# Performance work log

Measured on AMD Instinct MI355X. Metric: run time of the kernel, lower is better.

Reference implementation:

```python
import jax, jax.numpy as jnp
import numpy as np


def setup_inputs() -> dict:
    key = jax.random.key(0)
    k1, k2, k3, k4, k5, k6 = jax.random.split(key, 6)
    N, M = 4096, 4096      # data matrix
    K, D = 2048, 1024      # parameter matrix K x K, similarity matrix K x D
    Npair = 128            # size of i/j index subsets
    return {
        "actual": jax.random.normal(k1, (N, M), dtype=jnp.float32),
        "prediction": jax.random.normal(k2, (N, M), dtype=jnp.float32),
        "lamb": jnp.asarray(0.1, dtype=jnp.float32),
        "P": jax.random.normal(k3, (K, K), dtype=jnp.float32),
        "S": jax.random.normal(k4, (K, D), dtype=jnp.float32),
        "i_indices": jax.random.randint(k5, (Npair,), 0, K, dtype=jnp.int64),
        "j_indices": jax.random.randint(k6, (Npair,), 0, K, dtype=jnp.int64),
    }


def _safe_norm_rows(diff):
    # L2 norm over last axis with a zero-safe sqrt (grad is 0 at exactly-0 diffs,
    # matching torch's subgradient convention for .norm()).
    d2 = jnp.sum(diff * diff, axis=-1)
    pos = d2 > 0
    return jnp.sqrt(jnp.where(pos, d2, 1.0)) * pos


def reference(actual, prediction, lamb, P, S, i_indices, j_indices):
    # (p > 0) * clamp(p, min=0) == relu(p)
    Pp = jnp.maximum(P, 0.0)
    # penalty term: ||relu(P)||_F
    penalty = jnp.linalg.norm(Pp)
    # pairwise parameter-similarity penalty:
    # sum_{i in I, j in J} relu(P)[i,j] * || S[i,:] - S[j,:] ||_2
    Si = S[i_indices]                       # [Ni, D]
    Sj = S[j_indices]                       # [Nj, D]
    diff = Si[:, None, :] - Sj[None, :, :]  # [Ni, Nj, D]
    norms = _safe_norm_rows(diff)           # [Ni, Nj]
    Pij = Pp[i_indices[:, None], j_indices[None, :]]  # [Ni, Nj]
    parameter_penalty = jnp.sum(Pij * norms)
    data_term = jnp.linalg.norm(actual - prediction)
    return data_term + lamb * (penalty + parameter_penalty)
```

## Files before the change

kernel.cpp:

```cpp
#include <hip/hip_runtime.h>
#include <math.h>

#define BR 1024
#define BP 1024
#define TPB 256

__device__ __forceinline__ float waveReduceSum(float v) {
    #pragma unroll
    for (int off = 32; off > 0; off >>= 1)
        v += __shfl_down(v, off, 64);
    return v;
}

__global__ __launch_bounds__(256, 8)
void fused_kernel(const float* __restrict__ a,
                  const float* __restrict__ p,
                  const float* __restrict__ Pm,
                  const float* __restrict__ S,
                  const int* __restrict__ ii,
                  const int* __restrict__ jj,
                  float* __restrict__ ws,
                  long nAP, long nP, int Npair, int D, int K)
{
    __shared__ float sm0[4], sm1[4];
    const int wave = threadIdx.x >> 6;
    const int lane = threadIdx.x & 63;
    const int bid  = blockIdx.x;

    if (bid < BP) {
        const int totalPairs = Npair * Npair;
        int base = bid * 16 + wave * 4;
        float local = 0.f;
        #pragma unroll
        for (int q = 0; q < 4; ++q) {
            int pair = base + q;
            if (pair < totalPairs) {
                int i = pair / Npair;
                int j = pair - i * Npair;
                int ri = ii[i];
                int rj = jj[j];
                const float4* Si = (const float4*)(S + (long)ri * D);
                const float4* Sj = (const float4*)(S + (long)rj * D);
                float d2 = 0.f;
                int n4 = D >> 2;
                for (int k = lane; k < n4; k += 64) {
                    float4 x = Si[k];
                    float4 y = Sj[k];
                    float e0 = x.x - y.x;
                    float e1 = x.y - y.y;
                    float e2 = x.z - y.z;
                    float e3 = x.w - y.w;
                    d2 += e0*e0 + e1*e1 + e2*e2 + e3*e3;
                }
                d2 = waveReduceSum(d2);
                if (lane == 0 && d2 > 0.f)
                    local += fmaxf(Pm[(long)ri * K + rj], 0.f) * sqrtf(d2);
            }
        }
        if (lane == 0) sm0[wave] = local;
        __syncthreads();
        if (threadIdx.x == 0)
            ws[2 * BR + bid] = sm0[0] + sm0[1] + sm0[2] + sm0[3];
    } else {
        const int rb = bid - BP;
        const long tid    = (long)rb * TPB + threadIdx.x;
        const long stride = (long)BR * TPB;

        const float4* a4 = (const float4*)a;
        const float4* p4 = (const float4*)p;
        long n4 = nAP >> 2;

        float s0a = 0.f, s0b = 0.f, s0c = 0.f, s0d = 0.f;
        long i = tid;
        for (; i + 3 * stride < n4; i += 4 * stride) {
            float4 av0 = a4[i];
            float4 av1 = a4[i + stride];
            float4 av2 = a4[i + 2 * stride];
            float4 av3 = a4[i + 3 * stride];
            float4 pv0 = p4[i];
            float4 pv1 = p4[i + stride];
            float4 pv2 = p4[i + 2 * stride];
            float4 pv3 = p4[i + 3 * stride];
            {
                float d0 = av0.x - pv0.x, d1 = av0.y - pv0.y;
                float d2 = av0.z - pv0.z, d3 = av0.w - pv0.w;
                s0a += d0*d0 + d1*d1 + d2*d2 + d3*d3;
            }
            {
                float d0 = av1.x - pv1.x, d1 = av1.y - pv1.y;
                float d2 = av1.z - pv1.z, d3 = av1.w - pv1.w;
                s0b += d0*d0 + d1*d1 + d2*d2 + d3*d3;
            }
            {
                float d0 = av2.x - pv2.x, d1 = av2.y - pv2.y;
                float d2 = av2.z - pv2.z, d3 = av2.w - pv2.w;
                s0c += d0*d0 + d1*d1 + d2*d2 + d3*d3;
            }
            {
                float d0 = av3.x - pv3.x, d1 = av3.y - pv3.y;
                float d2 = av3.z - pv3.z, d3 = av3.w - pv3.w;
                s0d += d0*d0 + d1*d1 + d2*d2 + d3*d3;
            }
        }
        for (; i < n4; i += stride) {
            float4 av = a4[i];
            float4 pv = p4[i];
            float d0 = av.x - pv.x, d1 = av.y - pv.y;
            float d2 = av.z - pv.z, d3 = av.w - pv.w;
            s0a += d0*d0 + d1*d1 + d2*d2 + d3*d3;
        }

        const float4* P4 = (const float4*)Pm;
        long nP4 = nP >> 2;
        float s1a = 0.f, s1b = 0.f;
        i = tid;
        for (; i + stride < nP4; i += 2 * stride) {
            float4 v0 = P4[i];
            float4 v1 = P4[i + stride];
            {
                float r0 = fmaxf(v0.x, 0.f), r1 = fmaxf(v0.y, 0.f);
                float r2 = fmaxf(v0.z, 0.f), r3 = fmaxf(v0.w, 0.f);
                s1a += r0*r0 + r1*r1 + r2*r2 + r3*r3;
            }
            {
                float r0 = fmaxf(v1.x, 0.f), r1 = fmaxf(v1.y, 0.f);
                float r2 = fmaxf(v1.z, 0.f), r3 = fmaxf(v1.w, 0.f);
                s1b += r0*r0 + r1*r1 + r2*r2 + r3*r3;
            }
        }
        for (; i < nP4; i += stride) {
            float4 v = P4[i];
            float r0 = fmaxf(v.x, 0.f), r1 = fmaxf(v.y, 0.f);
            float r2 = fmaxf(v.z, 0.f), r3 = fmaxf(v.w, 0.f);
            s1a += r0*r0 + r1*r1 + r2*r2 + r3*r3;
        }

        float s0 = waveReduceSum(s0a + s0b + s0c + s0d);
        float s1 = waveReduceSum(s1a + s1b);
        if (lane == 0) { sm0[wave] = s0; sm1[wave] = s1; }
        __syncthreads();
        if (threadIdx.x == 0) {
            ws[rb]      = sm0[0] + sm0[1] + sm0[2] + sm0[3];
            ws[BR + rb] = sm1[0] + sm1[1] + sm1[2] + sm1[3];
        }
    }
}

__global__ void finalize_kernel(const float* __restrict__ ws,
                                const float* __restrict__ lamb,
                                float* __restrict__ out)
{
    float a0 = 0.f, a1 = 0.f, a2 = 0.f;
    for (int i = threadIdx.x; i < BR; i += TPB) {
        a0 += ws[i];
        a1 += ws[BR + i];
    }
    for (int i = threadIdx.x; i < BP; i += TPB)
        a2 += ws[2 * BR + i];

    a0 = waveReduceSum(a0);
    a1 = waveReduceSum(a1);
    a2 = waveReduceSum(a2);

    __shared__ float m0[4], m1[4], m2[4];
    int wave = threadIdx.x >> 6;
    int lane = threadIdx.x & 63;
    if (lane == 0) { m0[wave] = a0; m1[wave] = a1; m2[wave] = a2; }
    __syncthreads();
    if (threadIdx.x == 0) {
        float A0 = m0[0] + m0[1] + m0[2] + m0[3];
        float A1 = m1[0] + m1[1] + m1[2] + m1[3];
        float A2 = m2[0] + m2[1] + m2[2] + m2[3];
        out[0] = sqrtf(A0) + lamb[0] * (sqrtf(A1) + A2);
    }
}

extern "C" void kernel_launch(void* const* d_in, const int* in_sizes, int n_in,
                              void* d_out, int out_size, void* d_ws, size_t ws_size,
                              hipStream_t stream) {
    const float* actual = (const float*)d_in[0];
    const float* pred   = (const float*)d_in[1];
    const float* lamb   = (const float*)d_in[2];
    const float* Pm     = (const float*)d_in[3];
    const float* S      = (const float*)d_in[4];
    const int*   ii     = (const int*)d_in[5];
    const int*   jj     = (const int*)d_in[6];
    float* out = (float*)d_out;
    float* ws  = (float*)d_ws;

    long nAP   = in_sizes[0];
    long nP    = in_sizes[3];
    int  K     = (int)lround(sqrt((double)nP));
    int  Npair = in_sizes[5];
    int  D     = (int)(in_sizes[4] / K);

    fused_kernel<<<BP + BR, TPB, 0, stream>>>(actual, pred, Pm, S, ii, jj, ws,
                                              nAP, nP, Npair, D, K);
    finalize_kernel<<<1, TPB, 0, stream>>>(ws, lamb, out);
}
```

Measured before the change: 36.37 us.

## Stage Si rows in LDS for pair penalty and widen reduction grid

```diff
diff --git a/kernel.cpp b/kernel.cpp
--- a/kernel.cpp
+++ b/kernel.cpp
@@ -1,9 +1,9 @@
 #include <hip/hip_runtime.h>
 #include <math.h>
 
-#define BR 1024
-#define BP 1024
 #define TPB 256
+#define RB  4096
+#define TI  2
 
 __device__ __forceinline__ float waveReduceSum(float v) {
     #pragma unroll
@@ -12,7 +12,7 @@
     return v;
 }
 
-__global__ __launch_bounds__(256, 8)
+__global__ __launch_bounds__(TPB, 4)
 void fused_kernel(const float* __restrict__ a,
                   const float* __restrict__ p,
                   const float* __restrict__ Pm,
@@ -20,59 +20,77 @@
                   const int* __restrict__ ii,
                   const int* __restrict__ jj,
                   float* __restrict__ ws,
-                  long nAP, long nP, int Npair, int D, int K)
+                  long nAP, long nP, int Npair, int D, int K, int PBn)
 {
-    __shared__ float sm0[4], sm1[4];
     const int wave = threadIdx.x >> 6;
     const int lane = threadIdx.x & 63;
-    const int bid  = blockIdx.x;
-
-    if (bid < BP) {
-        const int totalPairs = Npair * Npair;
-        int base = bid * 16 + wave * 4;
+
+    if ((int)blockIdx.x < PBn) {
+        __shared__ float SiL[TI][1024];
+        __shared__ float psum[4];
+        const int i0 = blockIdx.x * TI;
+        const int n4 = D >> 2;
+
+        for (int idx = threadIdx.x; idx < TI * n4; idx += TPB) {
+            int r = idx / n4, c = idx - r * n4;
+            float4 v = make_float4(0.f, 0.f, 0.f, 0.f);
+            if (i0 + r < Npair)
+                v = ((const float4*)(S + (long)ii[i0 + r] * D))[c];
+            ((float4*)SiL[r])[c] = v;
+        }
+        __syncthreads();
+
+        const int ri0 = (i0     < Npair) ? ii[i0]     : 0;
+        const int ri1 = (i0 + 1 < Npair) ? ii[i0 + 1] : 0;
+
         float local = 0.f;
-        #pragma unroll
-        for (int q = 0; q < 4; ++q) {
-            int pair = base + q;
-            if (pair < totalPairs) {
-                int i = pair / Npair;
-                int j = pair - i * Npair;
-                int ri = ii[i];
-                int rj = jj[j];
-                const float4* Si = (const float4*)(S + (long)ri * D);
-                const float4* Sj = (const float4*)(S + (long)rj * D);
-                float d2 = 0.f;
-                int n4 = D >> 2;
-                for (int k = lane; k < n4; k += 64) {
-                    float4 x = Si[k];
-                    float4 y = Sj[k];
-                    float e0 = x.x - y.x;
-                    float e1 = x.y - y.y;
-                    float e2 = x.z - y.z;
-                    float e3 = x.w - y.w;
-                    d2 += e0*e0 + e1*e1 + e2*e2 + e3*e3;
-                }
-                d2 = waveReduceSum(d2);
-                if (lane == 0 && d2 > 0.f)
-                    local += fmaxf(Pm[(long)ri * K + rj], 0.f) * sqrtf(d2);
+        const int jPerWave = (Npair + 3) >> 2;
+        const int jb = wave * jPerWave;
+        const int je = min(Npair, jb + jPerWave);
+        for (int j = jb; j < je; ++j) {
+            const int rj = jj[j];
+            const float4* Sj = (const float4*)(S + (long)rj * D);
+            float d20 = 0.f, d21 = 0.f;
+            for (int c = lane; c < n4; c += 64) {
+                float4 y  = Sj[c];
+                float4 x0 = ((const float4*)SiL[0])[c];
+                float4 x1 = ((const float4*)SiL[1])[c];
+                float e;
+                e = x0.x - y.x; d20 += e * e;
+                e = x0.y - y.y; d20 += e * e;
+                e = x0.z - y.z; d20 += e * e;
+                e = x0.w - y.w; d20 += e * e;
+                e = x1.x - y.x; d21 += e * e;
+                e = x1.y - y.y; d21 += e * e;
+                e = x1.z - y.z; d21 += e * e;
+                e = x1.w - y.w; d21 += e * e;
             }
-        }
-        if (lane == 0) sm0[wave] = local;
+            d20 = waveReduceSum(d20);
+            d21 = waveReduceSum(d21);
+            if (lane == 0) {
+                if (i0     < Npair && d20 > 0.f)
+                    local += fmaxf(Pm[(long)ri0 * K + rj], 0.f) * sqrtf(d20);
+                if (i0 + 1 < Npair && d21 > 0.f)
+                    local += fmaxf(Pm[(long)ri1 * K + rj], 0.f) * sqrtf(d21);
+            }
+        }
+        if (lane == 0) psum[wave] = local;
         __syncthreads();
         if (threadIdx.x == 0)
-            ws[2 * BR + bid] = sm0[0] + sm0[1] + sm0[2] + sm0[3];
+            ws[2 * RB + blockIdx.x] = psum[0] + psum[1] + psum[2] + psum[3];
     } else {
-        const int rb = bid - BP;
-        const long tid    = (long)rb * TPB + threadIdx.x;
-        const long stride = (long)BR * TPB;
+        const int  rb     = blockIdx.x - PBn;
+        const long gtid   = (long)rb * TPB + threadIdx.x;
+        const long stride = (long)RB * TPB;
 
         const float4* a4 = (const float4*)a;
         const float4* p4 = (const float4*)p;
-        long n4 = nAP >> 2;
-
-        float s0a = 0.f, s0b = 0.f, s0c = 0.f, s0d = 0.f;
-        long i = tid;
-        for (; i + 3 * stride < n4; i += 4 * stride) {
+        const long n4  = nAP >> 2;
+        const long nP4 = nP  >> 2;
+
+        float s0 = 0.f, s1 = 0.f;
+        long i = gtid;
+        if (i + 3 * stride < n4) {
             float4 av0 = a4[i];
             float4 av1 = a4[i + stride];
             float4 av2 = a4[i + 2 * stride];
@@ -81,82 +99,68 @@
             float4 pv1 = p4[i + stride];
             float4 pv2 = p4[i + 2 * stride];
             float4 pv3 = p4[i + 3 * stride];
-            {
-                float d0 = av0.x - pv0.x, d1 = av0.y - pv0.y;
-                float d2 = av0.z - pv0.z, d3 = av0.w - pv0.w;
-                s0a += d0*d0 + d1*d1 + d2*d2 + d3*d3;
-            }
-            {
-                float d0 = av1.x - pv1.x, d1 = av1.y - pv1.y;
-                float d2 = av1.z - pv1.z, d3 = av1.w - pv1.w;
-                s0b += d0*d0 + d1*d1 + d2*d2 + d3*d3;
-            }
-            {
-                float d0 = av2.x - pv2.x, d1 = av2.y - pv2.y;
-                float d2 = av2.z - pv2.z, d3 = av2.w - pv2.w;
-                s0c += d0*d0 + d1*d1 + d2*d2 + d3*d3;
-            }
-            {
-                float d0 = av3.x - pv3.x, d1 = av3.y - pv3.y;
-                float d2 = av3.z - pv3.z, d3 = av3.w - pv3.w;
-                s0d += d0*d0 + d1*d1 + d2*d2 + d3*d3;
-            }
+            float d;
+            d = av0.x - pv0.x; s0 += d * d;
+            d = av0.y - pv0.y; s0 += d * d;
+            d = av0.z - pv0.z; s0 += d * d;
+            d = av0.w - pv0.w; s0 += d * d;
+            d = av1.x - pv1.x; s0 += d * d;
+            d = av1.y - pv1.y; s0 += d * d;
+            d = av1.z - pv1.z; s0 += d * d;
+            d = av1.w - pv1.w; s0 += d * d;
+            d = av2.x - pv2.x; s0 += d * d;
+            d = av2.y - pv2.y; s0 += d * d;
+            d = av2.z - pv2.z; s0 += d * d;
+            d = av2.w - pv2.w; s0 += d * d;
+            d = av3.x - pv3.x; s0 += d * d;
+            d = av3.y - pv3.y; s0 += d * d;
+            d = av3.z - pv3.z; s0 += d * d;
+            d = av3.w - pv3.w; s0 += d * d;
+            i += 4 * stride;
         }
         for (; i < n4; i += stride) {
-            float4 av = a4[i];
-            float4 pv = p4[i];
-            float d0 = av.x - pv.x, d1 = av.y - pv.y;
-            float d2 = av.z - pv.z, d3 = av.w - pv.w;
-            s0a += d0*d0 + d1*d1 + d2*d2 + d3*d3;
-        }
-
-        const float4* P4 = (const float4*)Pm;
-        long nP4 = nP >> 2;
-        float s1a = 0.f, s1b = 0.f;
-        i = tid;
-        for (; i + stride < nP4; i += 2 * stride) {
-            float4 v0 = P4[i];
-            float4 v1 = P4[i + stride];
-            {
-                float r0 = fmaxf(v0.x, 0.f), r1 = fmaxf(v0.y, 0.f);
-                float r2 = fmaxf(v0.z, 0.f), r3 = fmaxf(v0.w, 0.f);
-                s1a += r0*r0 + r1*r1 + r2*r2 + r3*r3;
-            }
-            {
-                float r0 = fmaxf(v1.x, 0.f), r1 = fmaxf(v1.y, 0.f);
-                float r2 = fmaxf(v1.z, 0.f), r3 = fmaxf(v1.w, 0.f);
-                s1b += r0*r0 + r1*r1 + r2*r2 + r3*r3;
-            }
-        }
-        for (; i < nP4; i += stride) {
-            float4 v = P4[i];
-            float r0 = fmaxf(v.x, 0.f), r1 = fmaxf(v.y, 0.f);
-            float r2 = fmaxf(v.z, 0.f), r3 = fmaxf(v.w, 0.f);
-            s1a += r0*r0 + r1*r1 + r2*r2 + r3*r3;
-        }
-
-        float s0 = waveReduceSum(s0a + s0b + s0c + s0d);
-        float s1 = waveReduceSum(s1a + s1b);
+            float4 av = a4[i], pv = p4[i];
+            float d;
+            d = av.x - pv.x; s0 += d * d;
+            d = av.y - pv.y; s0 += d * d;
+            d = av.z - pv.z; s0 += d * d;
+            d = av.w - pv.w; s0 += d * d;
+        }
+        for (long q = gtid; q < nP4; q += stride) {
+            float4 v = ((const float4*)Pm)[q];
+            float r;
+            r = fmaxf(v.x, 0.f); s1 += r * r;
+            r = fmaxf(v.y, 0.f); s1 += r * r;
+            r = fmaxf(v.z, 0.f); s1 += r * r;
+            r = fmaxf(v.w, 0.f); s1 += r * r;
+        }
+
+        s0 = waveReduceSum(s0);
+        s1 = waveReduceSum(s1);
+        __shared__ float sm0[4], sm1[4];
         if (lane == 0) { sm0[wave] = s0; sm1[wave] = s1; }
         __syncthreads();
         if (threadIdx.x == 0) {
             ws[rb]      = sm0[0] + sm0[1] + sm0[2] + sm0[3];
-            ws[BR + rb] = sm1[0] + sm1[1] + sm1[2] + sm1[3];
+            ws[RB + rb] = sm1[0] + sm1[1] + sm1[2] + sm1[3];
         }
     }
 }
 
 __global__ void finalize_kernel(const float* __restrict__ ws,
                                 const float* __restrict__ lamb,
-                                float* __restrict__ out)
+                                float* __restrict__ out, int PBn)
 {
     float a0 = 0.f, a1 = 0.f, a2 = 0.f;
-    for (int i = threadIdx.x; i < BR; i += TPB) {
-        a0 += ws[i];
-        a1 += ws[BR + i];
+    const float4* w4 = (const float4*)ws;
+    for (int i = threadIdx.x; i < RB / 4; i += TPB) {
+        float4 v = w4[i];
+        a0 += v.x + v.y + v.z + v.w;
+        float4 u = w4[RB / 4 + i];
+        a1 += u.x + u.y + u.z + u.w;
     }
-    for (int i = threadIdx.x; i < BP; i += TPB)
-        a2 += ws[2 * BR + i];
+    for (int i = threadIdx.x; i < PBn; i += TPB)
+        a2 += ws[2 * RB + i];
 
     a0 = waveReduceSum(a0);
     a1 = waveReduceSum(a1);
@@ -194,7 +198,9 @@
     int  Npair = in_sizes[5];
     int  D     = (int)(in_sizes[4] / K);
 
-    fused_kernel<<<BP + BR, TPB, 0, stream>>>(actual, pred, Pm, S, ii, jj, ws,
-                                              nAP, nP, Npair, D, K);
-    finalize_kernel<<<1, TPB, 0, stream>>>(ws, lamb, out);
-}
+    int PBn = (Npair + TI - 1) / TI;
+
+    fused_kernel<<<PBn + RB, TPB, 0, stream>>>(actual, pred, Pm, S, ii, jj, ws,
+                                               nAP, nP, Npair, D, K, PBn);
+    finalize_kernel<<<1, TPB, 0, stream>>>(ws, lamb, out, PBn);
+}
```

Measured after the change: 88.08 us. 142% more time.
